# Kernel optimization log

Measured on AMD Instinct MI355X. Metric: run time of the kernel, lower is better.

The kernel has to match this reference:

```python
import jax, jax.numpy as jnp
import numpy as np

B, S, D, H, E, K = 4, 2048, 1024, 2048, 8, 2
GH = max(D // 2, 32)  # 512 gating hidden


def setup_inputs() -> dict:
    key = jax.random.key(0)
    ks = jax.random.split(key, 16)
    def xav(k, shape):
        fan_in, fan_out = shape[0], shape[1]
        lim = (6.0 / (fan_in + fan_out)) ** 0.5
        return jax.random.uniform(k, shape, jnp.float32, -lim, lim)
    return {
        'x': jax.random.normal(ks[0], (B, S, D), jnp.float32),
        'feature_types': jax.random.randint(ks[1], (B, S), 0, 3),
        'gw1': xav(ks[2], (D, GH)), 'gb1': jnp.zeros((GH,), jnp.float32),
        'gw2': xav(ks[3], (GH, GH // 2)), 'gb2': jnp.zeros((GH // 2,), jnp.float32),
        'gw3': xav(ks[4], (GH // 2, E)), 'gb3': jnp.zeros((E,), jnp.float32),
        'type_emb': jax.random.normal(ks[5], (3, GH // 4), jnp.float32),
        'tw': xav(ks[6], (GH // 4, E)), 'tb': jnp.zeros((E,), jnp.float32),
        'ew': jax.random.normal(ks[7], (E, D, H), jnp.float32) * (1.0 / D ** 0.5),
        'eb': jnp.zeros((E, H), jnp.float32),
        'ow': xav(ks[8], (H, D)), 'ob': jnp.zeros((D,), jnp.float32),
    }


def reference(x, feature_types, gw1, gb1, gw2, gb2, gw3, gb3, type_emb, tw, tb, ew, eb, ow, ob):
    # Gating network (eval mode: dropout = identity)
    h = jax.nn.relu(x @ gw1 + gb1)
    h = jax.nn.relu(h @ gw2 + gb2)
    gate_logits = h @ gw3 + gb3                      # [B,S,E]
    type_bias = type_emb[feature_types] @ tw + tb    # [B,S,E]
    gate_weights = jax.nn.softmax(gate_logits + type_bias, axis=-1)

    # Top-k routing, renormalize selected weights
    expert_weights, expert_indices = jax.lax.top_k(gate_weights, K)  # [B,S,K]
    expert_weights = expert_weights / expert_weights.sum(-1, keepdims=True)

    # Dense expert compute (faithful to original: every expert on every token)
    expert_outputs = jnp.einsum('bsd,edh->bseh', x, ew) + eb         # [B,S,E,H]

    # Gather selected experts and combine
    sel = jnp.take_along_axis(expert_outputs, expert_indices[..., None], axis=2)  # [B,S,K,H]
    output = jnp.sum(expert_weights[..., None] * sel, axis=2)        # [B,S,H]

    output = jax.nn.relu(output)
    return output @ ow + ob                                          # [B,S,D]
```

## Files before the change

### kernel.cpp

```cpp
#include <hip/hip_runtime.h>

#define T_TOK 8192
#define DDIM 1024
#define GH1 512
#define GH2 256
#define NEXP 8
#define HDIM 2048

typedef __attribute__((ext_vector_type(8))) short short8;
typedef __attribute__((ext_vector_type(4))) float f32x4;

__device__ __forceinline__ unsigned short f2bf(float f) {
    unsigned int u = __float_as_uint(f);
    u += 0x7fffu + ((u >> 16) & 1u);
    return (unsigned short)(u >> 16);
}
__device__ __forceinline__ float bf2f(unsigned short h) {
    return __uint_as_float(((unsigned int)h) << 16);
}

__device__ __forceinline__ void async16(const void* g, void* l) {
#if __has_builtin(__builtin_amdgcn_global_load_lds)
    __builtin_amdgcn_global_load_lds((const __attribute__((address_space(1))) void*)g,
                                     (__attribute__((address_space(3))) void*)l, 16, 0, 0);
#else
    *(uint4*)l = *(const uint4*)g;
#endif
}

__global__ __launch_bounds__(256)
void f2b_kernel(const float* __restrict__ in, unsigned short* __restrict__ out)
{
    size_t i = ((size_t)blockIdx.x * 256 + threadIdx.x) * 8;
    float4 a = *(const float4*)(in + i);
    float4 b = *(const float4*)(in + i + 4);
    uint4 r;
    r.x = (unsigned)f2bf(a.x) | ((unsigned)f2bf(a.y) << 16);
    r.y = (unsigned)f2bf(a.z) | ((unsigned)f2bf(a.w) << 16);
    r.z = (unsigned)f2bf(b.x) | ((unsigned)f2bf(b.y) << 16);
    r.w = (unsigned)f2bf(b.z) | ((unsigned)f2bf(b.w) << 16);
    *(uint4*)(out + i) = r;
}

__global__ __launch_bounds__(256)
void transpose_f2b(const float* __restrict__ in, unsigned short* __restrict__ out,
                   int R, int C, int tilesC, int ntile)
{
    int bid = blockIdx.x;
    int z = bid / ntile;
    int r = bid - z * ntile;
    int tr = r / tilesC, tc = r - tr * tilesC;
    const float* ib = in + (size_t)z * R * C;
    unsigned short* ob = out + (size_t)z * R * C;
    __shared__ float lds[32][33];
    int t = threadIdx.x;
    int i = t >> 3, j4 = (t & 7) << 2;
    float4 v = *(const float4*)(ib + (size_t)(tr * 32 + i) * C + tc * 32 + j4);
    lds[i][j4 + 0] = v.x;
    lds[i][j4 + 1] = v.y;
    lds[i][j4 + 2] = v.z;
    lds[i][j4 + 3] = v.w;
    __syncthreads();
    ushort4 o;
    o.x = f2bf(lds[j4 + 0][i]);
    o.y = f2bf(lds[j4 + 1][i]);
    o.z = f2bf(lds[j4 + 2][i]);
    o.w = f2bf(lds[j4 + 3][i]);
    *(ushort4*)(ob + (size_t)(tc * 32 + i) * R + tr * 32 + j4) = o;
}

__global__ __launch_bounds__(256)
void sgemm_relu(const float* __restrict__ A, const float* __restrict__ B,
                const float* __restrict__ bias, float* __restrict__ C,
                int N, int Kd, int nbn)
{
    int bid = blockIdx.x;
    int bm = bid / nbn, bn = bid - bm * nbn;
    __shared__ float As[16][64];
    __shared__ float Bs[16][64];
    int t = threadIdx.x;
    int tx = t & 15, ty = t >> 4;
    float acc[4][4];
#pragma unroll
    for (int i = 0; i < 4; ++i)
#pragma unroll
        for (int j = 0; j < 4; ++j) acc[i][j] = 0.f;

    int arow = t >> 2, akk = (t & 3) << 2;
    int bkk = t >> 4, bcol = (t & 15) << 2;
    const float* aptr = A + (size_t)(bm * 64 + arow) * Kd + akk;
    const float* bptr = B + (size_t)bkk * N + bn * 64 + bcol;

    for (int k0 = 0; k0 < Kd; k0 += 16) {
        float4 av = *(const float4*)(aptr + k0);
        float4 bv = *(const float4*)(bptr + (size_t)k0 * N);
        __syncthreads();
        As[akk + 0][arow] = av.x;
        As[akk + 1][arow] = av.y;
        As[akk + 2][arow] = av.z;
        As[akk + 3][arow] = av.w;
        *(float4*)&Bs[bkk][bcol] = bv;
        __syncthreads();
#pragma unroll
        for (int kk = 0; kk < 16; ++kk) {
            float a[4], b[4];
            *(float4*)&a[0] = *(const float4*)&As[kk][ty * 4];
            *(float4*)&b[0] = *(const float4*)&Bs[kk][tx * 4];
#pragma unroll
            for (int i = 0; i < 4; ++i)
#pragma unroll
                for (int j = 0; j < 4; ++j)
                    acc[i][j] = fmaf(a[i], b[j], acc[i][j]);
        }
    }
#pragma unroll
    for (int i = 0; i < 4; ++i) {
        int row = bm * 64 + ty * 4 + i;
        float4 o;
        float* op = &o.x;
#pragma unroll
        for (int j = 0; j < 4; ++j) {
            int col = bn * 64 + tx * 4 + j;
            float v = acc[i][j] + bias[col];
            op[j] = v > 0.f ? v : 0.f;
        }
        *(float4*)&C[(size_t)row * N + bn * 64 + tx * 4] = o;
    }
}

__global__ __launch_bounds__(256)
void gate_tail(const float* __restrict__ h2, const int* __restrict__ ftyp,
               const float* __restrict__ gw3, const float* __restrict__ gb3,
               const float* __restrict__ temb, const float* __restrict__ tw,
               const float* __restrict__ tb,
               int* __restrict__ eidx, float* __restrict__ ewt)
{
    __shared__ float sw3[GH2 * NEXP];
    __shared__ float stw[128 * NEXP];
    __shared__ float ste[3 * 128];
    int t = threadIdx.x;
    for (int i = t; i < GH2 * NEXP; i += 256) sw3[i] = gw3[i];
    for (int i = t; i < 128 * NEXP; i += 256) stw[i] = tw[i];
    for (int i = t; i < 3 * 128; i += 256) ste[i] = temb[i];
    __syncthreads();
    int tok = blockIdx.x * 256 + t;
    float lg[NEXP];
#pragma unroll
    for (int e = 0; e < NEXP; ++e) lg[e] = gb3[e] + tb[e];
    const float* hrow = h2 + (size_t)tok * GH2;
    for (int k = 0; k < GH2; k += 4) {
        float4 hv = *(const float4*)(hrow + k);
        float hvv[4] = {hv.x, hv.y, hv.z, hv.w};
#pragma unroll
        for (int j = 0; j < 4; ++j) {
            float v = hvv[j];
#pragma unroll
            for (int e = 0; e < NEXP; ++e)
                lg[e] = fmaf(v, sw3[(k + j) * NEXP + e], lg[e]);
        }
    }
    int ft = ftyp[tok];
    const float* te = ste + ft * 128;
    for (int k = 0; k < 128; k += 4) {
#pragma unroll
        for (int j = 0; j < 4; ++j) {
            float v = te[k + j];
#pragma unroll
            for (int e = 0; e < NEXP; ++e)
                lg[e] = fmaf(v, stw[(k + j) * NEXP + e], lg[e]);
        }
    }
    int a0 = 0; float b0 = lg[0];
#pragma unroll
    for (int e = 1; e < NEXP; ++e) if (lg[e] > b0) { b0 = lg[e]; a0 = e; }
    int a1 = -1; float b1 = -3.4e38f;
#pragma unroll
    for (int e = 0; e < NEXP; ++e) if (e != a0 && lg[e] > b1) { b1 = lg[e]; a1 = e; }
    float w0 = 1.f / (1.f + expf(b1 - b0));
    eidx[tok * 2 + 0] = a0;
    eidx[tok * 2 + 1] = a1;
    ewt[tok * 2 + 0] = w0;
    ewt[tok * 2 + 1] = 1.f - w0;
}

__global__ __launch_bounds__(256)
void route_kernel(const int* __restrict__ eidx, int* __restrict__ cnt,
                  int* __restrict__ entries)
{
    int tok = blockIdx.x * 256 + threadIdx.x;
#pragma unroll
    for (int k = 0; k < 2; ++k) {
        int e = eidx[tok * 2 + k];
        int p = atomicAdd(&cnt[e], 1);
        entries[e * T_TOK + p] = (tok << 1) | k;
    }
}

template<int GATHER>
__global__ __launch_bounds__(256)
void bgemm(const unsigned short* __restrict__ A, const unsigned short* __restrict__ BT,
           const float* __restrict__ bias, float* __restrict__ Cf,
           unsigned short* __restrict__ Y0, unsigned short* __restrict__ Y1,
           const int* __restrict__ entries, const int* __restrict__ cnt,
           int N, int Kd, int nbm, int nbn)
{
    int bid = blockIdx.x;
    int e = 0, bm, bn, cntE = 0;
    const unsigned short* Bt = BT;
    const float* bs = bias;
    if (GATHER) {
        e = bid & (NEXP - 1);
        int r = bid >> 3;
        bm = r / nbn; bn = r - bm * nbn;
        cntE = cnt[e];
        if (bm * 128 >= cntE) return;
        Bt = BT + (size_t)e * HDIM * DDIM;
        bs = bias + e * HDIM;
    } else {
        bm = bid / nbn; bn = bid - bm * nbn;
    }

    __shared__ __align__(16) unsigned short As[2][128 * 32];
    __shared__ __align__(16) unsigned short Bs[2][128 * 32];
    __shared__ int rowtok[128];

    int t = threadIdx.x;
    if (GATHER) {
        if (t < 128) {
            int idx = bm * 128 + t;
            rowtok[t] = entries[(size_t)e * T_TOK + bm * 128 + ((idx < cntE) ? t : 0)];
        }
        __syncthreads();
    }

    int arow0 = t >> 2;
    int kkA = (t & 3) << 3;
    const unsigned short *asrc0, *asrc1;
    if (GATHER) {
        asrc0 = A + (size_t)(rowtok[arow0] >> 1) * Kd + kkA;
        asrc1 = A + (size_t)(rowtok[arow0 + 64] >> 1) * Kd + kkA;
    } else {
        asrc0 = A + (size_t)(bm * 128 + arow0) * Kd + kkA;
        asrc1 = A + (size_t)(bm * 128 + arow0 + 64) * Kd + kkA;
    }
    const unsigned short* bsrc0 = Bt + (size_t)(bn * 128 + arow0) * Kd + kkA;
    const unsigned short* bsrc1 = Bt + (size_t)(bn * 128 + arow0 + 64) * Kd + kkA;

    int lane = t & 63, wave = t >> 6;
    int wr = (wave >> 1) * 64, wc = (wave & 1) * 64;
    int l15 = lane & 15, lhi = lane >> 4;

    f32x4 zero = {0.f, 0.f, 0.f, 0.f};
    f32x4 acc[4][4];
#pragma unroll
    for (int m = 0; m < 4; ++m)
#pragma unroll
        for (int n = 0; n < 4; ++n) acc[m][n] = zero;

    async16(asrc0, &As[0][t * 8]);
    async16(asrc1, &As[0][t * 8 + 2048]);
    async16(bsrc0, &Bs[0][t * 8]);
    async16(bsrc1, &Bs[0][t * 8 + 2048]);
    __syncthreads();

    int nt = Kd >> 5;
    int cur = 0;
    for (int kt = 0; kt < nt; ++kt) {
        if (kt + 1 < nt) {
            int k0 = (kt + 1) << 5;
            int nb = cur ^ 1;
            async16(asrc0 + k0, &As[nb][t * 8]);
            async16(asrc1 + k0, &As[nb][t * 8 + 2048]);
            async16(bsrc0 + k0, &Bs[nb][t * 8]);
            async16(bsrc1 + k0, &Bs[nb][t * 8 + 2048]);
        }
        short8 af[4], bf[4];
#pragma unroll
        for (int m = 0; m < 4; ++m)
            af[m] = *(const short8*)&As[cur][(wr + m * 16 + l15) * 32 + lhi * 8];
#pragma unroll
        for (int n = 0; n < 4; ++n)
            bf[n] = *(const short8*)&Bs[cur][(wc + n * 16 + l15) * 32 + lhi * 8];
#pragma unroll
        for (int m = 0; m < 4; ++m)
#pragma unroll
            for (int n = 0; n < 4; ++n)
                acc[m][n] = __builtin_amdgcn_mfma_f32_16x16x32_bf16(af[m], bf[n], acc[m][n], 0, 0, 0);
        __syncthreads();
        cur ^= 1;
    }

    if (GATHER) {
#pragma unroll
        for (int m = 0; m < 4; ++m) {
            int rl = wr + m * 16 + lhi * 4;
#pragma unroll
            for (int q = 0; q < 4; ++q) {
                int gidx = bm * 128 + rl + q;
                if (gidx < cntE) {
                    int ent = rowtok[rl + q];
                    unsigned short* Y = (ent & 1) ? Y1 : Y0;
                    size_t rowoff = (size_t)(ent >> 1) * HDIM;
#pragma unroll
                    for (int n = 0; n < 4; ++n) {
                        int col = bn * 128 + wc + n * 16 + l15;
                        Y[rowoff + col] = f2bf(acc[m][n][q] + bs[col]);
                    }
                }
            }
        }
    } else {
#pragma unroll
        for (int m = 0; m < 4; ++m) {
            int row = bm * 128 + wr + m * 16 + lhi * 4;
#pragma unroll
            for (int n = 0; n < 4; ++n) {
                int col = bn * 128 + wc + n * 16 + l15;
                float bv = bs[col];
#pragma unroll
                for (int q = 0; q < 4; ++q)
                    Cf[(size_t)(row + q) * N + col] = acc[m][n][q] + bv;
            }
        }
    }
}

__global__ __launch_bounds__(256)
void combine_kernel(const unsigned short* __restrict__ Y0,
                    const unsigned short* __restrict__ Y1,
                    const float* __restrict__ wts,
                    unsigned short* __restrict__ Hc)
{
    size_t i = (size_t)blockIdx.x * 256 + threadIdx.x;
    size_t base = i * 8;
    int tok = (int)(base >> 11);
    float w0 = wts[tok * 2], w1 = wts[tok * 2 + 1];
    uint4 a = *(const uint4*)(Y0 + base);
    uint4 b = *(const uint4*)(Y1 + base);
    unsigned int ain[4] = {a.x, a.y, a.z, a.w};
    unsigned int bin[4] = {b.x, b.y, b.z, b.w};
    unsigned int r[4];
#pragma unroll
    for (int q = 0; q < 4; ++q) {
        float v0 = w0 * bf2f((unsigned short)(ain[q] & 0xffff)) +
                   w1 * bf2f((unsigned short)(bin[q] & 0xffff));
        float v1 = w0 * bf2f((unsigned short)(ain[q] >> 16)) +
                   w1 * bf2f((unsigned short)(bin[q] >> 16));
        v0 = v0 > 0.f ? v0 : 0.f;
        v1 = v1 > 0.f ? v1 : 0.f;
        r[q] = (unsigned int)f2bf(v0) | ((unsigned int)f2bf(v1) << 16);
    }
    uint4 o = {r[0], r[1], r[2], r[3]};
    *(uint4*)(Hc + base) = o;
}

extern "C" void kernel_launch(void* const* d_in, const int* in_sizes, int n_in,
                              void* d_out, int out_size, void* d_ws, size_t ws_size,
                              hipStream_t stream)
{
    const float* x    = (const float*)d_in[0];
    const int*   ftyp = (const int*)d_in[1];
    const float* gw1  = (const float*)d_in[2];
    const float* gb1  = (const float*)d_in[3];
    const float* gw2  = (const float*)d_in[4];
    const float* gb2  = (const float*)d_in[5];
    const float* gw3  = (const float*)d_in[6];
    const float* gb3  = (const float*)d_in[7];
    const float* temb = (const float*)d_in[8];
    const float* tw   = (const float*)d_in[9];
    const float* tb   = (const float*)d_in[10];
    const float* ew   = (const float*)d_in[11];
    const float* eb   = (const float*)d_in[12];
    const float* ow   = (const float*)d_in[13];
    const float* ob   = (const float*)d_in[14];
    float* out = (float*)d_out;

    char* p = (char*)d_ws;
    auto alloc = [&](size_t bytes) {
        char* r = p;
        p += (bytes + 255) & ~(size_t)255;
        return r;
    };
    unsigned short* xb  = (unsigned short*)alloc((size_t)T_TOK * DDIM * 2);
    float* h1           = (float*)alloc((size_t)T_TOK * GH1 * 4);
    float* h2           = (float*)alloc((size_t)T_TOK * GH2 * 4);
    int* eidx           = (int*)alloc((size_t)T_TOK * 2 * 4);
    float* ewt          = (float*)alloc((size_t)T_TOK * 2 * 4);
    int* cnt            = (int*)alloc(256);
    int* entries        = (int*)alloc((size_t)NEXP * T_TOK * 4);
    unsigned short* ewT = (unsigned short*)alloc((size_t)NEXP * HDIM * DDIM * 2);
    unsigned short* owT = (unsigned short*)alloc((size_t)DDIM * HDIM * 2);
    unsigned short* Y0  = (unsigned short*)alloc((size_t)T_TOK * HDIM * 2);
    unsigned short* Y1  = (unsigned short*)alloc((size_t)T_TOK * HDIM * 2);
    unsigned short* Hc  = (unsigned short*)alloc((size_t)T_TOK * HDIM * 2);

    hipMemsetAsync(cnt, 0, 256, stream);
    f2b_kernel<<<(T_TOK * DDIM / 8) / 256, 256, 0, stream>>>(x, xb);
    transpose_f2b<<<NEXP * 32 * 64, 256, 0, stream>>>(ew, ewT, DDIM, HDIM, 64, 32 * 64);
    transpose_f2b<<<64 * 32, 256, 0, stream>>>(ow, owT, HDIM, DDIM, 32, 64 * 32);

    sgemm_relu<<<128 * 8, 256, 0, stream>>>(x, gw1, gb1, h1, GH1, DDIM, 8);
    sgemm_relu<<<128 * 4, 256, 0, stream>>>(h1, gw2, gb2, h2, GH2, GH1, 4);
    gate_tail<<<T_TOK / 256, 256, 0, stream>>>(h2, ftyp, gw3, gb3, temb, tw, tb, eidx, ewt);
    route_kernel<<<T_TOK / 256, 256, 0, stream>>>(eidx, cnt, entries);

    bgemm<1><<<NEXP * 64 * 16, 256, 0, stream>>>(xb, ewT, eb, nullptr, Y0, Y1,
                                                 entries, cnt, HDIM, DDIM, 64, 16);
    combine_kernel<<<(T_TOK * HDIM / 8) / 256, 256, 0, stream>>>(Y0, Y1, ewt, Hc);
    bgemm<0><<<64 * 8, 256, 0, stream>>>(Hc, owT, ob, out, nullptr, nullptr,
                                         nullptr, nullptr, DDIM, HDIM, 64, 8);
}
```

Measured before the change: 670.5 us.

## Pipeline bf16 GEMM loads two stages ahead and enlarge first gating SGEMM tile

The MFMA GEMM now issues async global-to-LDS loads two K-tiles ahead, using explicit vmcnt/lgkmcnt waits and raw barriers instead of a full __syncthreads after each tile. This is meant to hide global load latency behind the MFMA work. Separately, the first fp32 gating GEMM switches to a 128x64 tile with 8x4 outputs per thread, which raises arithmetic intensity and halves the block count. The hand-written waitcnt logic is fragile and could race if the counts are wrong, and the larger tile uses more registers.

```diff
diff --git a/kernel.cpp b/kernel.cpp
--- a/kernel.cpp
+++ b/kernel.cpp
@@ -70,6 +70,70 @@
 }
 
 __global__ __launch_bounds__(256)
+void sgemm_relu_128x64(const float* __restrict__ A, const float* __restrict__ B,
+                       const float* __restrict__ bias, float* __restrict__ C,
+                       int N, int Kd, int nbn)
+{
+    int bid = blockIdx.x;
+    int bm = bid / nbn, bn = bid - bm * nbn;
+    __shared__ float As[16][128];
+    __shared__ float Bs[16][64];
+    int t = threadIdx.x;
+    int tx = t & 15, ty = t >> 4;
+    float acc[8][4];
+#pragma unroll
+    for (int i = 0; i < 8; ++i)
+#pragma unroll
+        for (int j = 0; j < 4; ++j) acc[i][j] = 0.f;
+
+    int arow = t >> 1, akk = (t & 1) << 3;
+    int bkk = t >> 4, bcol = (t & 15) << 2;
+    const float* aptr = A + (size_t)(bm * 128 + arow) * Kd + akk;
+    const float* bptr = B + (size_t)bkk * N + bn * 64 + bcol;
+
+    for (int k0 = 0; k0 < Kd; k0 += 16) {
+        float4 a0 = *(const float4*)(aptr + k0);
+        float4 a1 = *(const float4*)(aptr + k0 + 4);
+        float4 bv = *(const float4*)(bptr + (size_t)k0 * N);
+        __syncthreads();
+        As[akk + 0][arow] = a0.x;
+        As[akk + 1][arow] = a0.y;
+        As[akk + 2][arow] = a0.z;
+        As[akk + 3][arow] = a0.w;
+        As[akk + 4][arow] = a1.x;
+        As[akk + 5][arow] = a1.y;
+        As[akk + 6][arow] = a1.z;
+        As[akk + 7][arow] = a1.w;
+        *(float4*)&Bs[bkk][bcol] = bv;
+        __syncthreads();
+#pragma unroll
+        for (int kk = 0; kk < 16; ++kk) {
+            float a[8], b[4];
+            *(float4*)&a[0] = *(const float4*)&As[kk][ty * 8];
+            *(float4*)&a[4] = *(const float4*)&As[kk][ty * 8 + 4];
+            *(float4*)&b[0] = *(const float4*)&Bs[kk][tx * 4];
+#pragma unroll
+            for (int i = 0; i < 8; ++i)
+#pragma unroll
+                for (int j = 0; j < 4; ++j)
+                    acc[i][j] = fmaf(a[i], b[j], acc[i][j]);
+        }
+    }
+#pragma unroll
+    for (int i = 0; i < 8; ++i) {
+        int row = bm * 128 + ty * 8 + i;
+        float4 o;
+        float* op = &o.x;
+#pragma unroll
+        for (int j = 0; j < 4; ++j) {
+            float v = acc[i][j] + bias[bn * 64 + tx * 4 + j];
+            op[j] = v > 0.f ? v : 0.f;
+        }
+        *(float4*)&C[(size_t)row * N + bn * 64 + tx * 4] = o;
+    }
+}
+
+__global__ __launch_bounds__(256)
 void sgemm_relu(const float* __restrict__ A, const float* __restrict__ B,
                 const float* __restrict__ bias, float* __restrict__ C,
                 int N, int Kd, int nbn)
@@ -120,8 +184,7 @@
         float* op = &o.x;
 #pragma unroll
         for (int j = 0; j < 4; ++j) {
-            int col = bn * 64 + tx * 4 + j;
-            float v = acc[i][j] + bias[col];
+            float v = acc[i][j] + bias[bn * 64 + tx * 4 + j];
             op[j] = v > 0.f ? v : 0.f;
         }
         *(float4*)&C[(size_t)row * N + bn * 64 + tx * 4] = o;
@@ -257,23 +320,21 @@
 #pragma unroll
         for (int n = 0; n < 4; ++n) acc[m][n] = zero;
 
-    async16(asrc0, &As[0][t * 8]);
-    async16(asrc1, &As[0][t * 8 + 2048]);
-    async16(bsrc0, &Bs[0][t * 8]);
-    async16(bsrc1, &Bs[0][t * 8 + 2048]);
-    __syncthreads();
+    auto STAGE = [&](int buf, int k0) {
+        async16(asrc0 + k0, &As[buf][t * 8]);
+        async16(asrc1 + k0, &As[buf][t * 8 + 2048]);
+        async16(bsrc0 + k0, &Bs[buf][t * 8]);
+        async16(bsrc1 + k0, &Bs[buf][t * 8 + 2048]);
+    };
+
+    STAGE(0, 0);
+    STAGE(1, 32);
+    asm volatile("s_waitcnt vmcnt(4)" ::: "memory");
+    __builtin_amdgcn_s_barrier();
 
     int nt = Kd >> 5;
     int cur = 0;
     for (int kt = 0; kt < nt; ++kt) {
-        if (kt + 1 < nt) {
-            int k0 = (kt + 1) << 5;
-            int nb = cur ^ 1;
-            async16(asrc0 + k0, &As[nb][t * 8]);
-            async16(asrc1 + k0, &As[nb][t * 8 + 2048]);
-            async16(bsrc0 + k0, &Bs[nb][t * 8]);
-            async16(bsrc1 + k0, &Bs[nb][t * 8 + 2048]);
-        }
         short8 af[4], bf[4];
 #pragma unroll
         for (int m = 0; m < 4; ++m)
@@ -286,8 +347,18 @@
 #pragma unroll
             for (int n = 0; n < 4; ++n)
                 acc[m][n] = __builtin_amdgcn_mfma_f32_16x16x32_bf16(af[m], bf[n], acc[m][n], 0, 0, 0);
-        __syncthreads();
-        cur ^= 1;
+        if (kt + 1 < nt) {
+            asm volatile("s_waitcnt lgkmcnt(0)" ::: "memory");
+            __builtin_amdgcn_s_barrier();
+            if (kt + 2 < nt) {
+                STAGE(cur, (kt + 2) << 5);
+                asm volatile("s_waitcnt vmcnt(4)" ::: "memory");
+            } else {
+                asm volatile("s_waitcnt vmcnt(0)" ::: "memory");
+            }
+            __builtin_amdgcn_s_barrier();
+            cur ^= 1;
+        }
     }
 
     if (GATHER) {
@@ -399,7 +470,7 @@
     transpose_f2b<<<NEXP * 32 * 64, 256, 0, stream>>>(ew, ewT, DDIM, HDIM, 64, 32 * 64);
     transpose_f2b<<<64 * 32, 256, 0, stream>>>(ow, owT, HDIM, DDIM, 32, 64 * 32);
 
-    sgemm_relu<<<128 * 8, 256, 0, stream>>>(x, gw1, gb1, h1, GH1, DDIM, 8);
+    sgemm_relu_128x64<<<64 * 8, 256, 0, stream>>>(x, gw1, gb1, h1, GH1, DDIM, 8);
     sgemm_relu<<<128 * 4, 256, 0, stream>>>(h1, gw2, gb2, h2, GH2, GH1, 4);
     gate_tail<<<T_TOK / 256, 256, 0, stream>>>(h2, ftyp, gw3, gb3, temb, tw, tb, eidx, ewt);
     route_kernel<<<T_TOK / 256, 256, 0, stream>>>(eidx, cnt, entries);
```

Result: no change. 677.4 us (+1.0%).
